# Kernel optimization log

Measured on AMD Instinct MI355X. Metric: run time of the kernel, lower is better.

The kernel has to match this reference:

```python
import jax, jax.numpy as jnp
import numpy as np

N = 2048            # adj_size (num nodes)
F = 512             # in_features
M = 10              # m_chebyshev (polynomial order)
Q = 64              # Chebyshev-Gauss quadrature points for coefficients
HK_THRESHOLD = 1e-5 # args.hk_threshold


def setup_inputs() -> dict:
    key = jax.random.key(0)
    k1, k2 = jax.random.split(key, 2)
    x = jax.random.normal(k1, (N, F), dtype=jnp.float32)
    # random sparse symmetric adjacency -> normalized Laplacian P_n = I - D^-1/2 A D^-1/2
    u = jax.random.uniform(k2, (N, N), dtype=jnp.float32)
    a = (u < (16.0 / N)).astype(jnp.float32)
    a = jnp.maximum(a, a.T) * (1.0 - jnp.eye(N, dtype=jnp.float32))
    dinv = 1.0 / jnp.sqrt(jnp.clip(a.sum(1), 1.0, None))
    P_n = jnp.eye(N, dtype=jnp.float32) - dinv[:, None] * a * dinv[None, :]
    t = jnp.full((N,), -2.0, dtype=jnp.float32)  # Parameter init fill_(-2.0)
    eigmax = jnp.ones((1,), dtype=jnp.float32) * 2.0  # spectral bound of normalized Laplacian
    return {"x": x, "P_n": P_n, "t": t, "eigmax": eigmax}


def _cheb_coeffs(t, eigmax):
    # Per-node Chebyshev coefficients c[i,k] of exp(-exp(t_i) * lam),
    # lam = (eigmax/2)*(xhat+1), xhat in [-1,1]; computed with Chebyshev-Gauss
    # quadrature (numerically exact DCT form of the Bessel-function coefficients).
    s = jnp.exp(t)                                   # [N] per-node diffusion scale > 0
    theta = jnp.pi * (jnp.arange(Q, dtype=jnp.float32) + 0.5) / Q   # [Q]
    lam = (eigmax * 0.5) * (jnp.cos(theta) + 1.0)    # [Q] sampled eigenvalues
    w = jnp.exp(-s[:, None] * lam[None, :])          # [N,Q] exp(-s*lam)
    ck = jnp.cos(jnp.arange(M + 1, dtype=jnp.float32)[:, None] * theta[None, :])  # [M+1,Q]
    c = (2.0 / Q) * jnp.einsum('nq,kq->nk', w, ck)   # [N,M+1]
    return c.at[:, 0].mul(0.5)


def reference(x, P_n, t, eigmax):
    eigmax = eigmax.reshape(())
    c = _cheb_coeffs(t, eigmax)                       # [N,M+1]
    eye = jnp.eye(N, dtype=P_n.dtype)
    L_hat = (2.0 / eigmax) * P_n - eye                # scaled Laplacian, spectrum in [-1,1]
    # Chebyshev recurrence T_0=I, T_1=L_hat, T_k = 2 L_hat T_{k-1} - T_{k-2}
    T_prev, T_cur = eye, L_hat
    H = c[:, 0:1] * T_prev + c[:, 1:2] * T_cur        # per-row (per-node) coefficients
    for k in range(2, M + 1):
        T_prev, T_cur = T_cur, 2.0 * (L_hat @ T_cur) - T_prev
        H = H + c[:, k:k + 1] * T_cur
    H = jnp.where(H < HK_THRESHOLD, 0.0, H)           # hk[hk < hk_threshold] = 0
    output = H @ x                                    # [N,F]
    return output, t
```

## Files before the change

### kernel.cpp

```cpp
#include <hip/hip_runtime.h>
#include <hip/hip_fp16.h>

#define NN   2048
#define NF   512
#define MCH  10
#define QQ   64
#define KMAX 128
#define TOL  2e-3f
#define PI_F 3.14159265358979323846f

__device__ inline float2 h2f2(unsigned u) { return __half22float2(*(__half2*)&u); }
__device__ inline unsigned f2h2(float a, float b) {
    __half2 h = __floats2half2_rn(a, b);
    return *(unsigned*)&h;
}

__global__ __launch_bounds__(256) void xpose_in(const float* __restrict__ x,
                                                unsigned short* __restrict__ xT,
                                                float* __restrict__ pmax) {
    __shared__ float tile[64][65];
    __shared__ float wm[4];
    int r0 = blockIdx.x * 64;
    int f0 = blockIdx.y * 64;
    int tx = threadIdx.x & 63, ty = threadIdx.x >> 6;
    float m = 0.f;
#pragma unroll
    for (int i = 0; i < 16; ++i) {
        int rr = ty * 16 + i;
        float v = x[(size_t)(r0 + rr) * NF + f0 + tx];
        tile[rr][tx] = v;
        m = fmaxf(m, fabsf(v));
    }
    __syncthreads();
#pragma unroll
    for (int i = 0; i < 16; ++i) {
        int ff = ty * 16 + i;
        __half h = __float2half_rn(tile[tx][ff]);
        xT[(size_t)(f0 + ff) * NN + r0 + tx] = __half_as_ushort(h);
    }
#pragma unroll
    for (int o = 32; o > 0; o >>= 1) m = fmaxf(m, __shfl_down(m, o));
    if ((threadIdx.x & 63) == 0) wm[threadIdx.x >> 6] = m;
    __syncthreads();
    if (threadIdx.x == 0)
        pmax[blockIdx.y * 32 + blockIdx.x] = fmaxf(fmaxf(wm[0], wm[1]), fmaxf(wm[2], wm[3]));
}

__global__ __launch_bounds__(256) void csr_kernel(const float* __restrict__ P,
                                                  const float* __restrict__ eigmax,
                                                  const float* __restrict__ t,
                                                  unsigned* __restrict__ packed,
                                                  int* __restrict__ lens,
                                                  float* __restrict__ out) {
    int row = blockIdx.x;
    __shared__ int cnt;
    if (threadIdx.x == 0) cnt = 0;
    __syncthreads();
    float s2 = 2.0f / eigmax[0];
    for (int j = threadIdx.x; j < NN; j += 256) {
        float v = s2 * P[(size_t)row * NN + j] - (j == row ? 1.0f : 0.0f);
        if (v != 0.0f) {
            int p = atomicAdd(&cnt, 1);
            if (p < KMAX) {
                unsigned short hb = __half_as_ushort(__float2half_rn(v));
                packed[(size_t)p * NN + row] = ((unsigned)j << 20) | (unsigned)hb;
            }
        }
    }
    __syncthreads();
    if (threadIdx.x == 0) {
        lens[row] = min(cnt, KMAX);
        out[(size_t)NN * NF + row] = t[row];
    }
}

__global__ __launch_bounds__(1024) void cheb_fused(
    const unsigned short* __restrict__ xT, const float* __restrict__ t,
    const float* __restrict__ eigmax, const float* __restrict__ pmax,
    const unsigned* __restrict__ packed, const int* __restrict__ lens,
    float* __restrict__ outT) {
    __shared__ unsigned S[2][NN * 4];
    __shared__ float costab[QQ];
    __shared__ float redf[16];
    __shared__ int   redi[16];

    const int tid  = threadIdx.x;
    const int lane = tid & 63;
    const int wid  = tid >> 6;
    const int c0   = blockIdx.x * 2;
    const int r0   = tid;
    const int r1   = tid + 1024;

    if (tid < QQ) costab[tid] = cosf(PI_F * ((float)tid + 0.5f) / (float)QQ);

    float B = (tid < 256) ? pmax[tid] : 0.f;
#pragma unroll
    for (int o = 32; o > 0; o >>= 1) B = fmaxf(B, __shfl_down(B, o));
    if (lane == 0) redf[wid] = B;
    __syncthreads();
    B = redf[lane & 15];
#pragma unroll
    for (int o = 8; o > 0; o >>= 1) B = fmaxf(B, __shfl_down(B, o));
    B = __shfl(B, 0);
    const float bound = 45.2548f * B;

    const float em = eigmax[0];
    const float sA = expf(t[r0]);
    const float sB = expf(t[r1]);
    float cA[MCH + 1], cB[MCH + 1];
#pragma unroll
    for (int k = 0; k <= MCH; ++k) { cA[k] = 0.f; cB[k] = 0.f; }
    for (int q = 0; q < QQ; ++q) {
        float ct = costab[q];
        float lam = em * 0.5f * (ct + 1.0f);
        float wA = __expf(-sA * lam);
        float wB = __expf(-sB * lam);
        float pmA = 1.f, pcA = ct, pmB = 1.f, pcB = ct;
        cA[0] += wA;          cB[0] += wB;
        cA[1] += wA * ct;     cB[1] += wB * ct;
#pragma unroll
        for (int k = 2; k <= MCH; ++k) {
            float nA = 2.f * ct * pcA - pmA;
            float nB = 2.f * ct * pcB - pmB;
            cA[k] += wA * nA;  cB[k] += wB * nB;
            pmA = pcA; pcA = nA;
            pmB = pcB; pcB = nB;
        }
    }
#pragma unroll
    for (int k = 0; k <= MCH; ++k) {
        float sc = 2.0f / (float)QQ;
        cA[k] *= sc; cB[k] *= sc;
    }
    cA[0] *= 0.5f; cB[0] *= 0.5f;

    float tail0 = 0.f, tail1 = 0.f;
    int Ki = 1;
#pragma unroll
    for (int k = MCH; k >= 2; --k) {
        tail0 += fabsf(cA[k]);
        tail1 += fabsf(cB[k]);
        if (fmaxf(tail0, tail1) * bound > TOL) { Ki = k; break; }
    }
#pragma unroll
    for (int o = 32; o > 0; o >>= 1) Ki = max(Ki, __shfl_down(Ki, o));
    if (lane == 0) redi[wid] = Ki;
    __syncthreads();
    Ki = redi[lane & 15];
#pragma unroll
    for (int o = 8; o > 0; o >>= 1) Ki = max(Ki, __shfl_down(Ki, o));
    const int K = __shfl(Ki, 0);

    unsigned X0 = (unsigned)xT[(size_t)c0 * NN + r0] |
                  ((unsigned)xT[(size_t)(c0 + 1) * NN + r0] << 16);
    unsigned X1 = (unsigned)xT[(size_t)c0 * NN + r1] |
                  ((unsigned)xT[(size_t)(c0 + 1) * NN + r1] << 16);
    *(uint4*)&S[0][r0 * 4] = make_uint4(X0, X0, X0, X0);
    *(uint4*)&S[0][r1 * 4] = make_uint4(X1, X1, X1, X1);
    const int len0 = lens[r0];
    const int len1 = lens[r1];
    __syncthreads();

    const int laneoff = (tid & 3) * 4;
    auto gather = [&](int buf, int r, int len) -> unsigned {
        const char* Sb = (const char*)S[buf] + laneoff;
        unsigned accu = 0u;
        __half2 acc = *(__half2*)&accu;
#pragma unroll 8
        for (int e = 0; e < len; ++e) {
            unsigned pk = packed[(size_t)e * NN + r];
            unsigned g  = *(const unsigned*)(Sb + (pk >> 16));
            unsigned v2 = __builtin_amdgcn_perm(pk, pk, 0x01000100u);
            acc = __hfma2(*(__half2*)&v2, *(__half2*)&g, acc);
        }
        return *(unsigned*)&acc;
    };

    unsigned A0 = gather(0, r0, len0);
    unsigned A1 = gather(0, r1, len1);
    *(uint4*)&S[1][r0 * 4] = make_uint4(A0, A0, A0, A0);
    *(uint4*)&S[1][r1 * 4] = make_uint4(A1, A1, A1, A1);
    float2 xf0 = h2f2(X0), xf1 = h2f2(X1);
    float2 yf0 = h2f2(A0), yf1 = h2f2(A1);
    float2 H0 = make_float2(cA[0] * xf0.x + cA[1] * yf0.x, cA[0] * xf0.y + cA[1] * yf0.y);
    float2 H1 = make_float2(cB[0] * xf1.x + cB[1] * yf1.x, cB[0] * xf1.y + cB[1] * yf1.y);

    int cur = 1;
#pragma unroll
    for (int k = 2; k <= MCH; ++k) {
        if (k > K) break;
        __syncthreads();
        unsigned G0 = gather(cur, r0, len0);
        unsigned G1 = gather(cur, r1, len1);
        int oth = cur ^ 1;
        float2 gf0 = h2f2(G0), gf1 = h2f2(G1);
        float2 pf0 = h2f2(S[oth][r0 * 4]), pf1 = h2f2(S[oth][r1 * 4]);
        float2 t0 = make_float2(2.f * gf0.x - pf0.x, 2.f * gf0.y - pf0.y);
        float2 t1 = make_float2(2.f * gf1.x - pf1.x, 2.f * gf1.y - pf1.y);
        __syncthreads();
        unsigned T0 = f2h2(t0.x, t0.y), T1 = f2h2(t1.x, t1.y);
        *(uint4*)&S[oth][r0 * 4] = make_uint4(T0, T0, T0, T0);
        *(uint4*)&S[oth][r1 * 4] = make_uint4(T1, T1, T1, T1);
        H0.x += cA[k] * t0.x; H0.y += cA[k] * t0.y;
        H1.x += cB[k] * t1.x; H1.y += cB[k] * t1.y;
        cur = oth;
    }

    outT[(size_t)c0 * NN + r0]       = H0.x;
    outT[(size_t)(c0 + 1) * NN + r0] = H0.y;
    outT[(size_t)c0 * NN + r1]       = H1.x;
    outT[(size_t)(c0 + 1) * NN + r1] = H1.y;
}

__global__ __launch_bounds__(256) void xpose_out(const float* __restrict__ outT,
                                                 float* __restrict__ out) {
    __shared__ float tile[64][65];
    int f0 = blockIdx.x * 64;
    int r0 = blockIdx.y * 64;
    int tx = threadIdx.x & 63, ty = threadIdx.x >> 6;
#pragma unroll
    for (int i = 0; i < 16; ++i) {
        int ff = ty * 16 + i;
        tile[ff][tx] = outT[(size_t)(f0 + ff) * NN + r0 + tx];
    }
    __syncthreads();
#pragma unroll
    for (int i = 0; i < 16; ++i) {
        int rr = ty * 16 + i;
        out[(size_t)(r0 + rr) * NF + f0 + tx] = tile[tx][rr];
    }
}

extern "C" void kernel_launch(void* const* d_in, const int* in_sizes, int n_in,
                              void* d_out, int out_size, void* d_ws, size_t ws_size,
                              hipStream_t stream) {
    const float* x      = (const float*)d_in[0];
    const float* P_n    = (const float*)d_in[1];
    const float* t      = (const float*)d_in[2];
    const float* eigmax = (const float*)d_in[3];
    float* out = (float*)d_out;

    char* p = (char*)d_ws;
    auto carve = [&](size_t bytes) -> void* {
        void* r = (void*)p;
        p += (bytes + 255) & ~(size_t)255;
        return r;
    };
    unsigned*       packed = (unsigned*)      carve((size_t)KMAX * NN * sizeof(unsigned));
    int*            lens   = (int*)           carve((size_t)NN * sizeof(int));
    float*          pmax   = (float*)         carve((size_t)256 * sizeof(float));
    unsigned short* xT     = (unsigned short*)carve((size_t)NF * NN * sizeof(unsigned short));
    float*          outT   = (float*)         carve((size_t)NF * NN * sizeof(float));

    xpose_in<<<dim3(NN / 64, NF / 64), dim3(256), 0, stream>>>(x, xT, pmax);
    csr_kernel<<<dim3(NN), dim3(256), 0, stream>>>(P_n, eigmax, t, packed, lens, out);
    cheb_fused<<<dim3(NF / 2), dim3(1024), 0, stream>>>(xT, t, eigmax, pmax,
                                                        packed, lens, outT);
    xpose_out<<<dim3(NF / 64, NN / 64), dim3(256), 0, stream>>>(outT, out);
}
```

Baseline: 121.2 us.

## Precompute Chebyshev coefficients once per node and shrink shared-memory vector copies

Chebyshev coefficient computation moves out of cheb_fused, where each of 256 blocks recomputed all 2048 nodes' 64-point quadrature, into the CSR-building kernel. There each row computes its coefficients once with a wave reduction and stores them column-major. The shared-memory vectors in cheb_fused are also shrunk from 4 replicated copies per row to a single copy, with the packed column index shift changed to byte offsets accordingly. This cuts LDS to 16KB, which may allow more blocks per CU, at the cost of possible bank conflicts on gathers.

```diff
diff --git a/kernel.cpp b/kernel.cpp
--- a/kernel.cpp
+++ b/kernel.cpp
@@ -46,24 +46,56 @@
         pmax[blockIdx.y * 32 + blockIdx.x] = fmaxf(fmaxf(wm[0], wm[1]), fmaxf(wm[2], wm[3]));
 }
 
-__global__ __launch_bounds__(256) void csr_kernel(const float* __restrict__ P,
-                                                  const float* __restrict__ eigmax,
-                                                  const float* __restrict__ t,
-                                                  unsigned* __restrict__ packed,
-                                                  int* __restrict__ lens,
-                                                  float* __restrict__ out) {
+__global__ __launch_bounds__(256) void csr_coeff(const float* __restrict__ P,
+                                                 const float* __restrict__ eigmax,
+                                                 const float* __restrict__ t,
+                                                 unsigned* __restrict__ packed,
+                                                 int* __restrict__ lens,
+                                                 float* __restrict__ cc_cm,
+                                                 float* __restrict__ out) {
     int row = blockIdx.x;
     __shared__ int cnt;
     if (threadIdx.x == 0) cnt = 0;
     __syncthreads();
-    float s2 = 2.0f / eigmax[0];
+    float em = eigmax[0];
+    float s2 = 2.0f / em;
     for (int j = threadIdx.x; j < NN; j += 256) {
         float v = s2 * P[(size_t)row * NN + j] - (j == row ? 1.0f : 0.0f);
         if (v != 0.0f) {
             int p = atomicAdd(&cnt, 1);
             if (p < KMAX) {
                 unsigned short hb = __half_as_ushort(__float2half_rn(v));
-                packed[(size_t)p * NN + row] = ((unsigned)j << 20) | (unsigned)hb;
+                packed[(size_t)p * NN + row] = ((unsigned)j << 18) | (unsigned)hb;
+            }
+        }
+    }
+    if (threadIdx.x < QQ) {
+        int q = threadIdx.x;
+        float th = PI_F * ((float)q + 0.5f) / (float)QQ;
+        float ct = cosf(th);
+        float s  = expf(t[row]);
+        float w  = __expf(-s * em * 0.5f * (ct + 1.0f));
+        float tk[MCH + 1];
+        tk[0] = w;
+        tk[1] = w * ct;
+        float pm = 1.f, pc = ct;
+#pragma unroll
+        for (int k = 2; k <= MCH; ++k) {
+            float nx = 2.f * ct * pc - pm;
+            tk[k] = w * nx;
+            pm = pc; pc = nx;
+        }
+#pragma unroll
+        for (int o = 32; o > 0; o >>= 1) {
+#pragma unroll
+            for (int k = 0; k <= MCH; ++k) tk[k] += __shfl_down(tk[k], o);
+        }
+        if (q == 0) {
+#pragma unroll
+            for (int k = 0; k <= MCH; ++k) {
+                float v = tk[k] * (2.0f / (float)QQ);
+                if (k == 0) v *= 0.5f;
+                cc_cm[k * NN + row] = v;
             }
         }
     }
@@ -75,12 +107,11 @@
 }
 
 __global__ __launch_bounds__(1024) void cheb_fused(
-    const unsigned short* __restrict__ xT, const float* __restrict__ t,
-    const float* __restrict__ eigmax, const float* __restrict__ pmax,
+    const unsigned short* __restrict__ xT, const float* __restrict__ pmax,
+    const float* __restrict__ cc_cm,
     const unsigned* __restrict__ packed, const int* __restrict__ lens,
     float* __restrict__ outT) {
-    __shared__ unsigned S[2][NN * 4];
-    __shared__ float costab[QQ];
+    __shared__ unsigned S[2][NN];
     __shared__ float redf[16];
     __shared__ int   redi[16];
 
@@ -91,7 +122,12 @@
     const int r0   = tid;
     const int r1   = tid + 1024;
 
-    if (tid < QQ) costab[tid] = cosf(PI_F * ((float)tid + 0.5f) / (float)QQ);
+    float cA[MCH + 1], cB[MCH + 1];
+#pragma unroll
+    for (int k = 0; k <= MCH; ++k) {
+        cA[k] = cc_cm[k * NN + r0];
+        cB[k] = cc_cm[k * NN + r1];
+    }
 
     float B = (tid < 256) ? pmax[tid] : 0.f;
 #pragma unroll
@@ -103,36 +139,6 @@
     for (int o = 8; o > 0; o >>= 1) B = fmaxf(B, __shfl_down(B, o));
     B = __shfl(B, 0);
     const float bound = 45.2548f * B;
-
-    const float em = eigmax[0];
-    const float sA = expf(t[r0]);
-    const float sB = expf(t[r1]);
-    float cA[MCH + 1], cB[MCH + 1];
-#pragma unroll
-    for (int k = 0; k <= MCH; ++k) { cA[k] = 0.f; cB[k] = 0.f; }
-    for (int q = 0; q < QQ; ++q) {
-        float ct = costab[q];
-        float lam = em * 0.5f * (ct + 1.0f);
-        float wA = __expf(-sA * lam);
-        float wB = __expf(-sB * lam);
-        float pmA = 1.f, pcA = ct, pmB = 1.f, pcB = ct;
-        cA[0] += wA;          cB[0] += wB;
-        cA[1] += wA * ct;     cB[1] += wB * ct;
-#pragma unroll
-        for (int k = 2; k <= MCH; ++k) {
-            float nA = 2.f * ct * pcA - pmA;
-            float nB = 2.f * ct * pcB - pmB;
-            cA[k] += wA * nA;  cB[k] += wB * nB;
-            pmA = pcA; pcA = nA;
-            pmB = pcB; pcB = nB;
-        }
-    }
-#pragma unroll
-    for (int k = 0; k <= MCH; ++k) {
-        float sc = 2.0f / (float)QQ;
-        cA[k] *= sc; cB[k] *= sc;
-    }
-    cA[0] *= 0.5f; cB[0] *= 0.5f;
 
     float tail0 = 0.f, tail1 = 0.f;
     int Ki = 1;
@@ -155,15 +161,14 @@
                   ((unsigned)xT[(size_t)(c0 + 1) * NN + r0] << 16);
     unsigned X1 = (unsigned)xT[(size_t)c0 * NN + r1] |
                   ((unsigned)xT[(size_t)(c0 + 1) * NN + r1] << 16);
-    *(uint4*)&S[0][r0 * 4] = make_uint4(X0, X0, X0, X0);
-    *(uint4*)&S[0][r1 * 4] = make_uint4(X1, X1, X1, X1);
+    S[0][r0] = X0;
+    S[0][r1] = X1;
     const int len0 = lens[r0];
     const int len1 = lens[r1];
     __syncthreads();
 
-    const int laneoff = (tid & 3) * 4;
     auto gather = [&](int buf, int r, int len) -> unsigned {
-        const char* Sb = (const char*)S[buf] + laneoff;
+        const char* Sb = (const char*)S[buf];
         unsigned accu = 0u;
         __half2 acc = *(__half2*)&accu;
 #pragma unroll 8
@@ -178,8 +183,8 @@
 
     unsigned A0 = gather(0, r0, len0);
     unsigned A1 = gather(0, r1, len1);
-    *(uint4*)&S[1][r0 * 4] = make_uint4(A0, A0, A0, A0);
-    *(uint4*)&S[1][r1 * 4] = make_uint4(A1, A1, A1, A1);
+    S[1][r0] = A0;
+    S[1][r1] = A1;
     float2 xf0 = h2f2(X0), xf1 = h2f2(X1);
     float2 yf0 = h2f2(A0), yf1 = h2f2(A1);
     float2 H0 = make_float2(cA[0] * xf0.x + cA[1] * yf0.x, cA[0] * xf0.y + cA[1] * yf0.y);
@@ -194,13 +199,12 @@
         unsigned G1 = gather(cur, r1, len1);
         int oth = cur ^ 1;
         float2 gf0 = h2f2(G0), gf1 = h2f2(G1);
-        float2 pf0 = h2f2(S[oth][r0 * 4]), pf1 = h2f2(S[oth][r1 * 4]);
+        float2 pf0 = h2f2(S[oth][r0]), pf1 = h2f2(S[oth][r1]);
         float2 t0 = make_float2(2.f * gf0.x - pf0.x, 2.f * gf0.y - pf0.y);
         float2 t1 = make_float2(2.f * gf1.x - pf1.x, 2.f * gf1.y - pf1.y);
         __syncthreads();
-        unsigned T0 = f2h2(t0.x, t0.y), T1 = f2h2(t1.x, t1.y);
-        *(uint4*)&S[oth][r0 * 4] = make_uint4(T0, T0, T0, T0);
-        *(uint4*)&S[oth][r1 * 4] = make_uint4(T1, T1, T1, T1);
+        S[oth][r0] = f2h2(t0.x, t0.y);
+        S[oth][r1] = f2h2(t1.x, t1.y);
         H0.x += cA[k] * t0.x; H0.y += cA[k] * t0.y;
         H1.x += cB[k] * t1.x; H1.y += cB[k] * t1.y;
         cur = oth;
@@ -248,13 +252,13 @@
     };
     unsigned*       packed = (unsigned*)      carve((size_t)KMAX * NN * sizeof(unsigned));
     int*            lens   = (int*)           carve((size_t)NN * sizeof(int));
+    float*          cc_cm  = (float*)         carve((size_t)(MCH + 1) * NN * sizeof(float));
     float*          pmax   = (float*)         carve((size_t)256 * sizeof(float));
     unsigned short* xT     = (unsigned short*)carve((size_t)NF * NN * sizeof(unsigned short));
     float*          outT   = (float*)         carve((size_t)NF * NN * sizeof(float));
 
     xpose_in<<<dim3(NN / 64, NF / 64), dim3(256), 0, stream>>>(x, xT, pmax);
-    csr_kernel<<<dim3(NN), dim3(256), 0, stream>>>(P_n, eigmax, t, packed, lens, out);
-    cheb_fused<<<dim3(NF / 2), dim3(1024), 0, stream>>>(xT, t, eigmax, pmax,
-                                                        packed, lens, outT);
+    csr_coeff<<<dim3(NN), dim3(256), 0, stream>>>(P_n, eigmax, t, packed, lens, cc_cm, out);
+    cheb_fused<<<dim3(NF / 2), dim3(1024), 0, stream>>>(xT, pmax, cc_cm, packed, lens, outT);
     xpose_out<<<dim3(NF / 64, NN / 64), dim3(256), 0, stream>>>(outT, out);
 }
```

Result: faster. 107.6 us (-11.2%).
